# Kernel tuning notes

Measured on AMD Instinct MI355X. Metric: run time of the kernel, lower is better.

## Reference

```python
import jax, jax.numpy as jnp
import numpy as np

N_GROUPS = 4


def setup_inputs() -> dict:
    key = jax.random.key(0)
    ks = jax.random.split(key, 6)
    I, J, B = 512, 512, 4  # query tokens, key tokens, grid batch (B = 1 * n_groups)
    n_dim, out_per_group = 128, 4  # n_heads // n_groups = 16 // 4
    grid_q = jax.random.normal(ks[0], (I, 3), dtype=jnp.float32)
    grid_kv = jax.random.normal(ks[1], (B, J, 3), dtype=jnp.float32)
    W1 = jax.random.normal(ks[2], (3, n_dim), dtype=jnp.float32) * (1.0 / np.sqrt(3))
    b1 = jnp.zeros((n_dim,), dtype=jnp.float32)
    W2 = jax.random.normal(ks[3], (n_dim, n_dim), dtype=jnp.float32) * (1.0 / np.sqrt(n_dim))
    b2 = jnp.zeros((n_dim,), dtype=jnp.float32)
    W3 = jax.random.normal(ks[4], (n_dim, out_per_group), dtype=jnp.float32) * (1.0 / np.sqrt(n_dim))
    b3 = jnp.zeros((out_per_group,), dtype=jnp.float32)
    return {"grid_q": grid_q, "grid_kv": grid_kv, "W1": W1, "b1": b1,
            "W2": W2, "b2": b2, "W3": W3, "b3": b3}


def reference(grid_q, grid_kv, W1, b1, W2, b2, W3, b3):
    # grid_q: [I, 3] -> [1, I, 3]; grid_kv: [B, J, 3]
    gq = grid_q[None, :, :]
    # pairwise position difference: [B, I, J, 3]
    pos = gq[:, :, None, :] - grid_kv[:, None, :, :]
    # sign-log transform
    bias = jnp.sign(pos) * jnp.log1p(jnp.abs(pos))
    # tiny MLP: 3 -> n_dim -> n_dim -> heads//groups, pointwise over (B, I, J)
    h = jax.nn.relu(jnp.einsum('bijc,cd->bijd', bias, W1) + b1)
    h = jax.nn.relu(jnp.einsum('bijd,de->bije', h, W2) + b2)
    out = jnp.einsum('bije,eo->bijo', h, W3) + b3  # [B, I, J, O]
    # rearrange '(b g) i j o -> b (g o) i j' with g = N_GROUPS
    B, I, J, O = out.shape
    out = out.reshape(B // N_GROUPS, N_GROUPS, I, J, O)
    out = jnp.transpose(out, (0, 1, 4, 2, 3)).reshape(B // N_GROUPS, N_GROUPS * O, I, J)
    return out
```

## Files before the change

### kernel.cpp

```cpp
#include <hip/hip_runtime.h>
#include <math.h>

#define NBLOCKS 2048
#define THREADS 256
#define TILE 64
#define POS_PER_BLOCK 512
#define ITERS 8
#define CH 512

typedef __attribute__((ext_vector_type(8)))  short  short8;
typedef __attribute__((ext_vector_type(4)))  float  float4v;
typedef __attribute__((ext_vector_type(16))) float  float16;

__device__ __forceinline__ unsigned cvt_pk(float lo, float hi) {
    unsigned r;
    asm("v_cvt_pk_bf16_f32 %0, %1, %2" : "=v"(r) : "v"(lo), "v"(hi));
    return r;
}

__device__ __forceinline__ int kmap(int c, int jj) {
    return 32 * (c >> 2) + 16 * ((c >> 1) & 1) + 4 * (c & 1) + ((jj >> 2) << 3) + (jj & 3);
}

__global__ __launch_bounds__(256, 3)
void crpb_mfma8(const float* __restrict__ gq,
                const float* __restrict__ gkv,
                const float* __restrict__ W1,
                const float* __restrict__ b1,
                const float* __restrict__ W2,
                const float* __restrict__ b2,
                const float* __restrict__ W3,
                const float* __restrict__ b3,
                float* __restrict__ out)
{
    __shared__ __align__(16) unsigned short ash[2][16 * CH];
    __shared__ __align__(16) float red[2][2 * 4 * 64];
    __shared__ __align__(16) float b2s[128];

    const int tid  = threadIdx.x;
    const int lane = tid & 63;
    const int w    = __builtin_amdgcn_readfirstlane(tid >> 6);
    const int l31  = lane & 31;
    const int lh   = lane >> 5;

    if (tid < 128) b2s[tid] = b2[tid];

    const int ct2 = w & 1;
    const int ph  = w >> 1;
    const int pofs = ph * 32 + l31;

    float16 z16;
    #pragma unroll
    for (int r = 0; r < 16; ++r) z16[r] = 0.0f;

    short8 w1f[2];
    #pragma unroll
    for (int mt = 0; mt < 2; ++mt) {
        const int ch = (ct2 * 2 + mt) * 32 + l31;
        const float w0 = W1[ch], w1v = W1[128 + ch], w2v = W1[256 + ch], b1v = b1[ch];
        const float w0h = __uint_as_float(cvt_pk(w0, w0) << 16);
        const float w1h = __uint_as_float(cvt_pk(w1v, w1v) << 16);
        const float w2h = __uint_as_float(cvt_pk(w2v, w2v) << 16);
        const float b1h = __uint_as_float(cvt_pk(b1v, b1v) << 16);
        const float w0l = w0 - w0h, w1l = w1v - w1h, w2l = w2v - w2h, b1l = b1v - b1h;
        unsigned d[4];
        if (lh == 0) {
            d[0] = cvt_pk(w0h, w0l);
            d[1] = cvt_pk(w0h, w1h);
            d[2] = cvt_pk(w1l, w1h);
            d[3] = cvt_pk(w2h, w2l);
        } else {
            d[0] = cvt_pk(w2h, b1h);
            d[1] = cvt_pk(b1l, 0.0f);
            d[2] = 0; d[3] = 0;
        }
        __builtin_memcpy(&w1f[mt], d, 16);
    }

    short8 a2f[2][8];
    #pragma unroll
    for (int mt = 0; mt < 2; ++mt) {
        const int e = ct2 * 64 + mt * 32 + l31;
        #pragma unroll
        for (int ks = 0; ks < 8; ++ks) {
            const int c = 2 * ks + lh;
            unsigned t0[4];
            #pragma unroll
            for (int t = 0; t < 4; ++t) {
                const int d0 = kmap(c, 2 * t), d1 = d0 + 1;
                t0[t] = cvt_pk(W2[d0 * 128 + e], W2[d1 * 128 + e]);
            }
            __builtin_memcpy(&a2f[mt][ks], t0, 16);
        }
    }

    short8 w3a[2][2];
    #pragma unroll
    for (int mt = 0; mt < 2; ++mt) {
        #pragma unroll
        for (int m2 = 0; m2 < 2; ++m2) {
            unsigned tt[4];
            #pragma unroll
            for (int t = 0; t < 4; ++t) {
                const int chl = ((2 * t) & 3) + 8 * ((2 * t) >> 2) + 4 * lh + 16 * m2;
                const int ch0 = (ct2 * 2 + mt) * 32 + chl, ch1 = ch0 + 1;
                const float lo = (l31 < 4) ? W3[ch0 * 4 + l31] : 0.0f;
                const float hi = (l31 < 4) ? W3[ch1 * 4 + l31] : 0.0f;
                tt[t] = cvt_pk(lo, hi);
            }
            __builtin_memcpy(&w3a[mt][m2], tt, 16);
        }
    }
    const float b3r = b3[w];

    const int posblock = blockIdx.x * POS_PER_BLOCK;
    const int bb = posblock >> 18;
    const int i  = (posblock >> 9) & 511;
    const float q0 = gq[i * 3 + 0], q1 = gq[i * 3 + 1], q2 = gq[i * 3 + 2];
    const float* kvrow = gkv + (size_t)(bb << 9) * 3;

    const float* kp = kvrow + (size_t)pofs * 3;
    float kv0 = kp[0], kv1 = kp[1], kv2 = kp[2];

    auto phaseA = [&](int x, int buf) {
        const float c0 = q0 - kv0, c1 = q1 - kv1, c2 = q2 - kv2;
        const float* kn = kvrow + (size_t)((((x + 1) & 7) << 6) + pofs) * 3;
        kv0 = kn[0]; kv1 = kn[1]; kv2 = kn[2];

        const float f0 = copysignf(__logf(1.0f + fabsf(c0)), c0);
        const float f1 = copysignf(__logf(1.0f + fabsf(c1)), c1);
        const float f2 = copysignf(__logf(1.0f + fabsf(c2)), c2);
        const unsigned u0 = cvt_pk(f0, f0), u2 = cvt_pk(f2, f2);
        const float f0h = __uint_as_float(u0 << 16);
        const float f1h = __uint_as_float(cvt_pk(f1, f1) << 16);
        const float f2h = __uint_as_float(u2 << 16);
        const float f0l = f0 - f0h, f1l = f1 - f1h, f2l = f2 - f2h;

        unsigned d[4];
        if (lh == 0) {
            d[0] = u0;
            d[1] = cvt_pk(f0l, f1);
            d[2] = cvt_pk(f1, f1l);
            d[3] = u2;
        } else {
            d[0] = cvt_pk(f2l, 1.0f);
            d[1] = cvt_pk(1.0f, 0.0f);
            d[2] = 0; d[3] = 0;
        }
        short8 bf; __builtin_memcpy(&bf, d, 16);

        #pragma unroll
        for (int mt = 0; mt < 2; ++mt) {
            const int cti = ct2 * 2 + mt;
            float16 c1r = __builtin_amdgcn_mfma_f32_32x32x16_bf16(w1f[mt], bf, z16, 0, 0, 0);
            unsigned pk0[4], pk1[4];
            #pragma unroll
            for (int t = 0; t < 4; ++t) {
                pk0[t] = cvt_pk(fmaxf(c1r[2 * t], 0.f),     fmaxf(c1r[2 * t + 1], 0.f));
                pk1[t] = cvt_pk(fmaxf(c1r[8 + 2 * t], 0.f), fmaxf(c1r[8 + 2 * t + 1], 0.f));
            }
            short8 v0, v1;
            __builtin_memcpy(&v0, pk0, 16);
            __builtin_memcpy(&v1, pk1, 16);
            *(short8*)&ash[buf][(4 * cti + lh) * CH + pofs * 8]     = v0;
            *(short8*)&ash[buf][(4 * cti + 2 + lh) * CH + pofs * 8] = v1;
        }
    };

    phaseA(0, 0);
    __syncthreads();

    for (int it = 0; it < ITERS; ++it) {
        const int buf = it & 1;
        const int jb = it * TILE;

        float16 acc0, acc1;
        #pragma unroll
        for (int qr = 0; qr < 4; ++qr) {
            float4v i0 = *(const float4v*)&b2s[(ct2 * 2 + 0) * 32 + 8 * qr + 4 * lh];
            float4v i1 = *(const float4v*)&b2s[(ct2 * 2 + 1) * 32 + 8 * qr + 4 * lh];
            #pragma unroll
            for (int t = 0; t < 4; ++t) { acc0[4 * qr + t] = i0[t]; acc1[4 * qr + t] = i1[t]; }
        }
        const unsigned short* br = &ash[buf][lh * CH + pofs * 8];
        #pragma unroll
        for (int ks = 0; ks < 8; ++ks) {
            short8 bfrag = *(const short8*)(br + ks * 2 * CH);
            acc0 = __builtin_amdgcn_mfma_f32_32x32x16_bf16(a2f[0][ks], bfrag, acc0, 0, 0, 0);
            acc1 = __builtin_amdgcn_mfma_f32_32x32x16_bf16(a2f[1][ks], bfrag, acc1, 0, 0, 0);
        }

        {
            unsigned pa0[4], pa1[4], pb0[4], pb1[4];
            #pragma unroll
            for (int t = 0; t < 4; ++t) {
                pa0[t] = cvt_pk(fmaxf(acc0[2 * t], 0.f),     fmaxf(acc0[2 * t + 1], 0.f));
                pa1[t] = cvt_pk(fmaxf(acc0[8 + 2 * t], 0.f), fmaxf(acc0[8 + 2 * t + 1], 0.f));
                pb0[t] = cvt_pk(fmaxf(acc1[2 * t], 0.f),     fmaxf(acc1[2 * t + 1], 0.f));
                pb1[t] = cvt_pk(fmaxf(acc1[8 + 2 * t], 0.f), fmaxf(acc1[8 + 2 * t + 1], 0.f));
            }
            short8 fa0, fa1, fb0, fb1;
            __builtin_memcpy(&fa0, pa0, 16); __builtin_memcpy(&fa1, pa1, 16);
            __builtin_memcpy(&fb0, pb0, 16); __builtin_memcpy(&fb1, pb1, 16);
            float16 p;
            p = __builtin_amdgcn_mfma_f32_32x32x16_bf16(w3a[0][0], fa0, z16, 0, 0, 0);
            p = __builtin_amdgcn_mfma_f32_32x32x16_bf16(w3a[0][1], fa1, p, 0, 0, 0);
            p = __builtin_amdgcn_mfma_f32_32x32x16_bf16(w3a[1][0], fb0, p, 0, 0, 0);
            p = __builtin_amdgcn_mfma_f32_32x32x16_bf16(w3a[1][1], fb1, p, 0, 0, 0);
            if (lh == 0) {
                #pragma unroll
                for (int o = 0; o < 4; ++o)
                    red[buf][ct2 * 256 + o * 64 + pofs] = p[o];
            }
        }

        if (it != ITERS - 1) phaseA(it + 1, 1 - buf);

        __syncthreads();

        {
            const int o = w, pos = lane;
            const float v = b3r + red[buf][o * 64 + pos] + red[buf][256 + o * 64 + pos];
            out[((size_t)((bb << 2) + o) << 18) + ((size_t)i << 9) + jb + pos] = v;
        }
    }
}

extern "C" void kernel_launch(void* const* d_in, const int* in_sizes, int n_in,
                              void* d_out, int out_size, void* d_ws, size_t ws_size,
                              hipStream_t stream) {
    const float* gq  = (const float*)d_in[0];
    const float* gkv = (const float*)d_in[1];
    const float* W1  = (const float*)d_in[2];
    const float* b1  = (const float*)d_in[3];
    const float* W2  = (const float*)d_in[4];
    const float* b2  = (const float*)d_in[5];
    const float* W3  = (const float*)d_in[6];
    const float* b3  = (const float*)d_in[7];
    float* out = (float*)d_out;

    crpb_mfma8<<<NBLOCKS, THREADS, 0, stream>>>(gq, gkv, W1, b1, W2, b2, W3, b3, out);
}
```

Baseline: 122.2 us.

## Keep layer-1 activations in registers and feed layer-2 MFMA directly, drop LDS staging

Each wave now computes all 128 layer-1 channels for its 32 positions and repacks the accumulator straight into layer-2 B fragments, removing the LDS round trip and the per-iteration barrier. The b2 bias is folded into an extra MFMA against a constant-ones fragment, and output reduction is deferred to a single barrier after all iterations. This duplicates layer-1 MFMA work across the two channel-half waves and raises register pressure, with launch bounds lowered from 3 to 2 blocks per SM.

```diff
diff --git a/kernel.cpp b/kernel.cpp
--- a/kernel.cpp
+++ b/kernel.cpp
@@ -4,12 +4,10 @@
 #define NBLOCKS 2048
 #define THREADS 256
 #define TILE 64
+#define ITERS 8
 #define POS_PER_BLOCK 512
-#define ITERS 8
-#define CH 512
 
 typedef __attribute__((ext_vector_type(8)))  short  short8;
-typedef __attribute__((ext_vector_type(4)))  float  float4v;
 typedef __attribute__((ext_vector_type(16))) float  float16;
 
 __device__ __forceinline__ unsigned cvt_pk(float lo, float hi) {
@@ -18,12 +16,8 @@
     return r;
 }
 
-__device__ __forceinline__ int kmap(int c, int jj) {
-    return 32 * (c >> 2) + 16 * ((c >> 1) & 1) + 4 * (c & 1) + ((jj >> 2) << 3) + (jj & 3);
-}
-
-__global__ __launch_bounds__(256, 3)
-void crpb_mfma8(const float* __restrict__ gq,
+__global__ __launch_bounds__(256, 2)
+void crpb_mfma9(const float* __restrict__ gq,
                 const float* __restrict__ gkv,
                 const float* __restrict__ W1,
                 const float* __restrict__ b1,
@@ -33,9 +27,7 @@
                 const float* __restrict__ b3,
                 float* __restrict__ out)
 {
-    __shared__ __align__(16) unsigned short ash[2][16 * CH];
-    __shared__ __align__(16) float red[2][2 * 4 * 64];
-    __shared__ __align__(16) float b2s[128];
+    __shared__ __align__(16) float red[ITERS][2][4][64];
 
     const int tid  = threadIdx.x;
     const int lane = tid & 63;
@@ -43,20 +35,18 @@
     const int l31  = lane & 31;
     const int lh   = lane >> 5;
 
-    if (tid < 128) b2s[tid] = b2[tid];
-
     const int ct2 = w & 1;
-    const int ph  = w >> 1;
-    const int pofs = ph * 32 + l31;
+    const int pg  = w >> 1;
+    const int pofs = pg * 32 + l31;
 
     float16 z16;
     #pragma unroll
     for (int r = 0; r < 16; ++r) z16[r] = 0.0f;
 
-    short8 w1f[2];
-    #pragma unroll
-    for (int mt = 0; mt < 2; ++mt) {
-        const int ch = (ct2 * 2 + mt) * 32 + l31;
+    short8 w1f[4];
+    #pragma unroll
+    for (int T = 0; T < 4; ++T) {
+        const int ch = 32 * T + l31;
         const float w0 = W1[ch], w1v = W1[128 + ch], w2v = W1[256 + ch], b1v = b1[ch];
         const float w0h = __uint_as_float(cvt_pk(w0, w0) << 16);
         const float w1h = __uint_as_float(cvt_pk(w1v, w1v) << 16);
@@ -74,44 +64,63 @@
             d[1] = cvt_pk(b1l, 0.0f);
             d[2] = 0; d[3] = 0;
         }
-        __builtin_memcpy(&w1f[mt], d, 16);
-    }
-
-    short8 a2f[2][8];
-    #pragma unroll
-    for (int mt = 0; mt < 2; ++mt) {
-        const int e = ct2 * 64 + mt * 32 + l31;
+        __builtin_memcpy(&w1f[T], d, 16);
+    }
+
+    short8 a2fT[2][8];
+    #pragma unroll
+    for (int ot = 0; ot < 2; ++ot) {
+        const int m = ct2 * 64 + ot * 32 + l31;
         #pragma unroll
         for (int ks = 0; ks < 8; ++ks) {
-            const int c = 2 * ks + lh;
             unsigned t0[4];
             #pragma unroll
             for (int t = 0; t < 4; ++t) {
-                const int d0 = kmap(c, 2 * t), d1 = d0 + 1;
-                t0[t] = cvt_pk(W2[d0 * 128 + e], W2[d1 * 128 + e]);
-            }
-            __builtin_memcpy(&a2f[mt][ks], t0, 16);
-        }
+                const int s  = 8 * lh + 2 * t;
+                const int d0 = 16 * ks + (s & 3) + 8 * ((s >> 2) & 1) + 4 * (s >> 3);
+                t0[t] = cvt_pk(W2[d0 * 128 + m], W2[(d0 + 1) * 128 + m]);
+            }
+            __builtin_memcpy(&a2fT[ot][ks], t0, 16);
+        }
+    }
+
+    short8 a2b2[2];
+    #pragma unroll
+    for (int ot = 0; ot < 2; ++ot) {
+        const int ch = ct2 * 64 + ot * 32 + l31;
+        const float b2v = b2[ch];
+        const float b2h = __uint_as_float(cvt_pk(b2v, b2v) << 16);
+        const float b2l = b2v - b2h;
+        unsigned d[4];
+        d[0] = (lh == 0) ? cvt_pk(b2h, b2l) : 0u;
+        d[1] = 0; d[2] = 0; d[3] = 0;
+        __builtin_memcpy(&a2b2[ot], d, 16);
+    }
+    short8 bconst;
+    {
+        unsigned d[4];
+        d[0] = (lh == 0) ? 0x3F803F80u : 0u;
+        d[1] = 0; d[2] = 0; d[3] = 0;
+        __builtin_memcpy(&bconst, d, 16);
     }
 
     short8 w3a[2][2];
     #pragma unroll
-    for (int mt = 0; mt < 2; ++mt) {
+    for (int ot = 0; ot < 2; ++ot) {
         #pragma unroll
         for (int m2 = 0; m2 < 2; ++m2) {
             unsigned tt[4];
             #pragma unroll
             for (int t = 0; t < 4; ++t) {
                 const int chl = ((2 * t) & 3) + 8 * ((2 * t) >> 2) + 4 * lh + 16 * m2;
-                const int ch0 = (ct2 * 2 + mt) * 32 + chl, ch1 = ch0 + 1;
+                const int ch0 = ct2 * 64 + ot * 32 + chl, ch1 = ch0 + 1;
                 const float lo = (l31 < 4) ? W3[ch0 * 4 + l31] : 0.0f;
                 const float hi = (l31 < 4) ? W3[ch1 * 4 + l31] : 0.0f;
                 tt[t] = cvt_pk(lo, hi);
             }
-            __builtin_memcpy(&w3a[mt][m2], tt, 16);
-        }
-    }
-    const float b3r = b3[w];
+            __builtin_memcpy(&w3a[ot][m2], tt, 16);
+        }
+    }
 
     const int posblock = blockIdx.x * POS_PER_BLOCK;
     const int bb = posblock >> 18;
@@ -122,9 +131,9 @@
     const float* kp = kvrow + (size_t)pofs * 3;
     float kv0 = kp[0], kv1 = kp[1], kv2 = kp[2];
 
-    auto phaseA = [&](int x, int buf) {
+    for (int it = 0; it < ITERS; ++it) {
         const float c0 = q0 - kv0, c1 = q1 - kv1, c2 = q2 - kv2;
-        const float* kn = kvrow + (size_t)((((x + 1) & 7) << 6) + pofs) * 3;
+        const float* kn = kvrow + (size_t)((((it + 1) & 7) << 6) + pofs) * 3;
         kv0 = kn[0]; kv1 = kn[1]; kv2 = kn[2];
 
         const float f0 = copysignf(__logf(1.0f + fabsf(c0)), c0);
@@ -149,45 +158,23 @@
         }
         short8 bf; __builtin_memcpy(&bf, d, 16);
 
-        #pragma unroll
-        for (int mt = 0; mt < 2; ++mt) {
-            const int cti = ct2 * 2 + mt;
-            float16 c1r = __builtin_amdgcn_mfma_f32_32x32x16_bf16(w1f[mt], bf, z16, 0, 0, 0);
-            unsigned pk0[4], pk1[4];
-            #pragma unroll
-            for (int t = 0; t < 4; ++t) {
-                pk0[t] = cvt_pk(fmaxf(c1r[2 * t], 0.f),     fmaxf(c1r[2 * t + 1], 0.f));
-                pk1[t] = cvt_pk(fmaxf(c1r[8 + 2 * t], 0.f), fmaxf(c1r[8 + 2 * t + 1], 0.f));
-            }
-            short8 v0, v1;
-            __builtin_memcpy(&v0, pk0, 16);
-            __builtin_memcpy(&v1, pk1, 16);
-            *(short8*)&ash[buf][(4 * cti + lh) * CH + pofs * 8]     = v0;
-            *(short8*)&ash[buf][(4 * cti + 2 + lh) * CH + pofs * 8] = v1;
-        }
-    };
-
-    phaseA(0, 0);
-    __syncthreads();
-
-    for (int it = 0; it < ITERS; ++it) {
-        const int buf = it & 1;
-        const int jb = it * TILE;
-
-        float16 acc0, acc1;
-        #pragma unroll
-        for (int qr = 0; qr < 4; ++qr) {
-            float4v i0 = *(const float4v*)&b2s[(ct2 * 2 + 0) * 32 + 8 * qr + 4 * lh];
-            float4v i1 = *(const float4v*)&b2s[(ct2 * 2 + 1) * 32 + 8 * qr + 4 * lh];
-            #pragma unroll
-            for (int t = 0; t < 4; ++t) { acc0[4 * qr + t] = i0[t]; acc1[4 * qr + t] = i1[t]; }
-        }
-        const unsigned short* br = &ash[buf][lh * CH + pofs * 8];
-        #pragma unroll
-        for (int ks = 0; ks < 8; ++ks) {
-            short8 bfrag = *(const short8*)(br + ks * 2 * CH);
-            acc0 = __builtin_amdgcn_mfma_f32_32x32x16_bf16(a2f[0][ks], bfrag, acc0, 0, 0, 0);
-            acc1 = __builtin_amdgcn_mfma_f32_32x32x16_bf16(a2f[1][ks], bfrag, acc1, 0, 0, 0);
+        float16 acc0 = __builtin_amdgcn_mfma_f32_32x32x16_bf16(a2b2[0], bconst, z16, 0, 0, 0);
+        float16 acc1 = __builtin_amdgcn_mfma_f32_32x32x16_bf16(a2b2[1], bconst, z16, 0, 0, 0);
+
+        #pragma unroll
+        for (int T = 0; T < 4; ++T) {
+            float16 c1r = __builtin_amdgcn_mfma_f32_32x32x16_bf16(w1f[T], bf, z16, 0, 0, 0);
+            #pragma unroll
+            for (int hi2 = 0; hi2 < 2; ++hi2) {
+                unsigned pk[4];
+                #pragma unroll
+                for (int t = 0; t < 4; ++t)
+                    pk[t] = cvt_pk(fmaxf(c1r[8 * hi2 + 2 * t], 0.f),
+                                   fmaxf(c1r[8 * hi2 + 2 * t + 1], 0.f));
+                short8 bf2; __builtin_memcpy(&bf2, pk, 16);
+                acc0 = __builtin_amdgcn_mfma_f32_32x32x16_bf16(a2fT[0][2 * T + hi2], bf2, acc0, 0, 0, 0);
+                acc1 = __builtin_amdgcn_mfma_f32_32x32x16_bf16(a2fT[1][2 * T + hi2], bf2, acc1, 0, 0, 0);
+            }
         }
 
         {
@@ -210,18 +197,21 @@
             if (lh == 0) {
                 #pragma unroll
                 for (int o = 0; o < 4; ++o)
-                    red[buf][ct2 * 256 + o * 64 + pofs] = p[o];
-            }
-        }
-
-        if (it != ITERS - 1) phaseA(it + 1, 1 - buf);
-
-        __syncthreads();
-
-        {
-            const int o = w, pos = lane;
-            const float v = b3r + red[buf][o * 64 + pos] + red[buf][256 + o * 64 + pos];
-            out[((size_t)((bb << 2) + o) << 18) + ((size_t)i << 9) + jb + pos] = v;
+                    red[it][ct2][o][pofs] = p[o];
+            }
+        }
+    }
+
+    __syncthreads();
+
+    {
+        const int o = tid >> 6, pos = tid & 63;
+        const float b3v = b3[o];
+        float* obase = out + ((size_t)((bb << 2) + o) << 18) + ((size_t)i << 9) + pos;
+        #pragma unroll
+        for (int it = 0; it < ITERS; ++it) {
+            const float v = b3v + red[it][0][o][pos] + red[it][1][o][pos];
+            obase[it * TILE] = v;
         }
     }
 }
@@ -239,5 +229,5 @@
     const float* b3  = (const float*)d_in[7];
     float* out = (float*)d_out;
 
-    crpb_mfma8<<<NBLOCKS, THREADS, 0, stream>>>(gq, gkv, W1, b1, W2, b2, W3, b3, out);
+    crpb_mfma9<<<NBLOCKS, THREADS, 0, stream>>>(gq, gkv, W1, b1, W2, b2, W3, b3, out);
 }
```

New measurement: 133.2 us. 1.09x slower.
